# Kernel optimization log

Hardware: AMD Instinct MI355X
Metric: run time of the kernel (lower is better)

## Reference

```python
import jax, jax.numpy as jnp
import numpy as np

B, S, D, H, F = 4, 4096, 1024, 16, 4096
CAP = 0.125
ROPE_BASE = 10000.0


def setup_inputs() -> dict:
    key = jax.random.key(0)
    ks = jax.random.split(key, 9)
    scale = 0.02
    x = jax.random.normal(ks[0], (B, S, D), jnp.float32)
    causal = jnp.where(jnp.tril(jnp.ones((S, S), bool)), 0.0, -1e9).astype(jnp.float32)
    attention_mask = jnp.broadcast_to(causal[None, None], (B, 1, S, S))
    position_ids = jnp.broadcast_to(jnp.arange(S, dtype=jnp.int32), (B, S))
    return {
        "x": x,
        "attention_mask": attention_mask,
        "position_ids": position_ids,
        "router_w": jax.random.normal(ks[1], (D, 1), jnp.float32) * scale,
        "router_b": jnp.zeros((1,), jnp.float32),
        "wq": jax.random.normal(ks[2], (D, D), jnp.float32) * scale,
        "wk": jax.random.normal(ks[3], (D, D), jnp.float32) * scale,
        "wv": jax.random.normal(ks[4], (D, D), jnp.float32) * scale,
        "wo": jax.random.normal(ks[5], (D, D), jnp.float32) * scale,
        "w1": jax.random.normal(ks[6], (D, F), jnp.float32) * scale,
        "w2": jax.random.normal(ks[7], (F, D), jnp.float32) * scale,
        "ln1": jnp.ones((D,), jnp.float32),
        "ln2": jnp.ones((D,), jnp.float32),
    }


def rmsnorm(x, g):
    return x * jax.lax.rsqrt(jnp.mean(x * x, -1, keepdims=True) + 1e-6) * g


def rope(t, pos):
    # t: [b, h, n, hd], pos: [b, n]
    hd = t.shape[-1]
    inv = 1.0 / (ROPE_BASE ** (jnp.arange(0, hd, 2, dtype=jnp.float32) / hd))
    f = pos[:, None, :, None].astype(jnp.float32) * inv  # [b,1,n,hd/2]
    emb = jnp.concatenate([f, f], axis=-1)
    cos, sin = jnp.cos(emb), jnp.sin(emb)
    rot = jnp.concatenate([-t[..., hd // 2:], t[..., : hd // 2]], axis=-1)
    return t * cos + rot * sin


def reference(x, attention_mask, position_ids, router_w, router_b,
              wq, wk, wv, wo, w1, w2, ln1, ln2):
    b, s, d = x.shape
    hd = d // H
    # router
    weights = (x @ router_w)[..., 0] + router_b[0]  # [b,s]
    k = int(CAP * s)
    topv, topi = jax.lax.top_k(weights, k)
    thr = topv[:, -1]
    sel_mask = (weights > thr[:, None]).astype(x.dtype)  # selects k-1 tokens/row
    kc = k - 1
    sel_idx = jnp.sort(topi[:, :kc], axis=1)  # preserve sequence order, [b,kc]
    bidx = jnp.arange(b)[:, None]
    # gather selected tokens / positions / weights
    x_sel = x[bidx, sel_idx]                 # [b,kc,d]
    pos_sel = position_ids[bidx, sel_idx]    # [b,kc]
    w_sel = weights[bidx, sel_idx]           # [b,kc]
    m = attention_mask[:, 0]                 # [b,s,s]
    m_sel = m[bidx[:, :, None], sel_idx[:, :, None], sel_idx[:, None, :]]  # [b,kc,kc]
    # transformer block on selected tokens
    hn = rmsnorm(x_sel, ln1)

    def heads(t):
        return t.reshape(b, kc, H, hd).transpose(0, 2, 1, 3)

    q = rope(heads(hn @ wq), pos_sel)
    kk = rope(heads(hn @ wk), pos_sel)
    v = heads(hn @ wv)
    sc = jnp.einsum('bhqd,bhkd->bhqk', q, kk) / np.sqrt(hd).astype(np.float32)
    sc = sc + m_sel[:, None]
    a = jax.nn.softmax(sc, axis=-1)
    o = jnp.einsum('bhqk,bhkd->bhqd', a, v).transpose(0, 2, 1, 3).reshape(b, kc, d) @ wo
    x1 = x_sel + o
    x2 = x1 + jax.nn.gelu(rmsnorm(x1, ln2) @ w1) @ w2
    # weighted scatter back + residual passthrough for unselected tokens
    proc = x2 * w_sel[..., None]
    out = jnp.zeros_like(x).at[bidx, sel_idx].set(proc)
    return out + x * (1.0 - sel_mask)[..., None]
```

## Files before the change

### kernel.cpp

```cpp
#include <hip/hip_runtime.h>

typedef __bf16 bf16;
typedef __bf16 bf16x8 __attribute__((ext_vector_type(8)));
typedef __bf16 bf16x4 __attribute__((ext_vector_type(4)));
typedef float f32x4 __attribute__((ext_vector_type(4)));

#define B_ 4
#define S_ 4096
#define D_ 1024
#define H_ 16
#define HD_ 64
#define F_ 4096
#define KC 512
#define M_ (B_ * KC)

#define GLDS16(gp, lp)                                                        \
    __builtin_amdgcn_global_load_lds(                                         \
        (const __attribute__((address_space(1))) void*)(gp),                  \
        (__attribute__((address_space(3))) void*)(lp), 16, 0, 0)

__global__ __launch_bounds__(256) void prep_kernel(const float* __restrict__ x,
                                                   const float* __restrict__ rw,
                                                   const float* __restrict__ rb,
                                                   float* __restrict__ weights,
                                                   const float* __restrict__ wq, bf16* __restrict__ wqT,
                                                   const float* __restrict__ wk, bf16* __restrict__ wkT,
                                                   const float* __restrict__ wv, bf16* __restrict__ wvT,
                                                   const float* __restrict__ wo, bf16* __restrict__ woT,
                                                   const float* __restrict__ w1, bf16* __restrict__ w1T,
                                                   const float* __restrict__ w2, bf16* __restrict__ w2T) {
    int bid = blockIdx.x;
    if (bid < 4096) {
        int wvv = threadIdx.x >> 6, lane = threadIdx.x & 63;
        int t = bid * 4 + wvv;
        const float* xr = x + (size_t)t * D_;
        float s = 0.f;
        for (int c = 0; c < 4; c++) {
            int off = c * 256 + lane * 4;
            float4 xv = *(const float4*)(xr + off);
            float4 wv4 = *(const float4*)(rw + off);
            s += xv.x * wv4.x + xv.y * wv4.y + xv.z * wv4.z + xv.w * wv4.w;
        }
        for (int m = 32; m; m >>= 1) s += __shfl_down(s, m);
        if (lane == 0) weights[t] = s + rb[0];
        return;
    }
    bid -= 4096;
    const float* in;
    bf16* out;
    int C, R, bx, by;
    if (bid < 1024)      { in = wq; out = wqT; C = 1024; R = 1024; bx = bid & 31; by = bid >> 5; }
    else if (bid < 2048) { int t = bid - 1024; in = wk; out = wkT; C = 1024; R = 1024; bx = t & 31; by = t >> 5; }
    else if (bid < 3072) { int t = bid - 2048; in = wv; out = wvT; C = 1024; R = 1024; bx = t & 31; by = t >> 5; }
    else if (bid < 4096) { int t = bid - 3072; in = wo; out = woT; C = 1024; R = 1024; bx = t & 31; by = t >> 5; }
    else if (bid < 8192) { int t = bid - 4096; in = w1; out = w1T; C = 4096; R = 1024; bx = t & 127; by = t >> 7; }
    else                 { int t = bid - 8192; in = w2; out = w2T; C = 1024; R = 4096; bx = t & 31; by = t >> 5; }
    __shared__ bf16 tile[32][33];
    int tx = threadIdx.x & 31, ty = threadIdx.x >> 5;
    int c0 = bx * 32, r0 = by * 32;
    for (int k = 0; k < 4; k++)
        tile[ty + k * 8][tx] = (bf16)in[(size_t)(r0 + ty + k * 8) * C + c0 + tx];
    __syncthreads();
    for (int k = 0; k < 4; k++)
        out[(size_t)(c0 + ty + k * 8) * R + r0 + tx] = tile[tx][ty + k * 8];
}

__global__ __launch_bounds__(1024) void topk_kernel(const float* __restrict__ weights,
                                                    const int* __restrict__ pos_ids,
                                                    int* __restrict__ sel_idx,
                                                    float* __restrict__ w_sel,
                                                    float* __restrict__ possel,
                                                    float* __restrict__ thr,
                                                    int* __restrict__ invmap) {
    __shared__ unsigned ords[S_];
    __shared__ unsigned hist[16][256];
    __shared__ unsigned wscan[16];
    __shared__ unsigned found[2];
    int b = blockIdx.x, tid = threadIdx.x, wv = tid >> 6, lane = tid & 63;
    const float* wb = weights + (size_t)b * S_;
    for (int i = tid; i < S_; i += 1024) {
        unsigned bits = __float_as_uint(wb[i]);
        ords[i] = (bits & 0x80000000u) ? ~bits : (bits | 0x80000000u);
        invmap[b * S_ + i] = -1;
    }
    unsigned pref = 0, pmask = 0;
    int rank = 512;
    for (int level = 0; level < 4; level++) {
        int shift = 24 - level * 8;
        for (int i = tid; i < 16 * 256; i += 1024) (&hist[0][0])[i] = 0;
        __syncthreads();
        for (int i = tid; i < S_; i += 1024) {
            unsigned o = ords[i];
            if ((o & pmask) == pref) atomicAdd(&hist[wv][(o >> shift) & 255], 1u);
        }
        __syncthreads();
        unsigned val = 0, v = 0;
        if (tid < 256) {
            unsigned s = 0;
            for (int w = 0; w < 16; w++) s += hist[w][255 - tid];
            val = s;
            v = s;
            for (int d = 1; d < 64; d <<= 1) {
                unsigned u = __shfl_up(v, d);
                if (lane >= d) v += u;
            }
            if (lane == 63) wscan[wv] = v;
        }
        __syncthreads();
        if (tid < 256) {
            unsigned woff = 0;
            for (int w = 0; w < wv; w++) woff += wscan[w];
            unsigned Ccnt = v + woff;
            if (val > 0 && Ccnt >= (unsigned)rank && Ccnt - val < (unsigned)rank) {
                found[0] = 255 - (unsigned)tid;
                found[1] = Ccnt - val;
            }
        }
        __syncthreads();
        pref |= found[0] << shift;
        pmask |= 0xffu << shift;
        rank -= (int)found[1];
        __syncthreads();
    }
    unsigned T = pref;
    int need_eq = rank - 1;
    unsigned cnt = 0;
    int i0 = tid * 4;
    unsigned o4[4];
    for (int k = 0; k < 4; k++) {
        unsigned o = ords[i0 + k];
        o4[k] = o;
        cnt += (o > T) ? 1u : 0u;
        cnt += (o == T) ? 0x10000u : 0u;
    }
    unsigned v2 = cnt;
    for (int d = 1; d < 64; d <<= 1) {
        unsigned u = __shfl_up(v2, d);
        if (lane >= d) v2 += u;
    }
    if (lane == 63) wscan[wv] = v2;
    __syncthreads();
    unsigned woff2 = 0;
    for (int w = 0; w < wv; w++) woff2 += wscan[w];
    unsigned excl = woff2 + v2 - cnt;
    unsigned gbe = excl & 0xffffu, ebe = excl >> 16;
    for (int k = 0; k < 4; k++) {
        unsigned o = o4[k];
        bool gt = o > T, eq = (o == T);
        if (gt || (eq && ebe < (unsigned)need_eq)) {
            unsigned esel = (ebe < (unsigned)need_eq) ? ebe : (unsigned)need_eq;
            unsigned pos = gbe + esel;
            sel_idx[b * KC + pos] = i0 + k;
            w_sel[b * KC + pos] = wb[i0 + k];
            possel[b * KC + pos] = (float)pos_ids[b * S_ + i0 + k];
            invmap[b * S_ + i0 + k] = (int)pos;
        }
        gbe += gt ? 1u : 0u;
        ebe += eq ? 1u : 0u;
    }
    if (tid == 0) {
        unsigned bits = (T & 0x80000000u) ? (T & 0x7fffffffu) : ~T;
        thr[b] = __uint_as_float(bits);
        sel_idx[b * KC + 511] = 0;
        w_sel[b * KC + 511] = 0.0f;
        possel[b * KC + 511] = 0.0f;
    }
}

__global__ __launch_bounds__(256) void gather_norm_kernel(const float* __restrict__ x,
                                                          const int* __restrict__ sel_idx,
                                                          const float* __restrict__ ln1,
                                                          bf16* __restrict__ hn) {
    int r = blockIdx.x, b = r >> 9, j = r & (KC - 1);
    int tid = threadIdx.x;
    bf16* outr = hn + (size_t)r * D_;
    if (j == 511) {
        ((uint2*)outr)[tid] = make_uint2(0u, 0u);
        return;
    }
    int idx = sel_idx[r];
    const float* xr = x + ((size_t)b * S_ + idx) * D_;
    float4 xv = ((const float4*)xr)[tid];
    float v[4] = {xv.x, xv.y, xv.z, xv.w}, ss = 0.f;
    for (int i = 0; i < 4; i++) ss += v[i] * v[i];
    __shared__ float red[4];
    float t = ss;
    for (int m = 32; m; m >>= 1) t += __shfl_down(t, m);
    if ((tid & 63) == 0) red[tid >> 6] = t;
    __syncthreads();
    ss = red[0] + red[1] + red[2] + red[3];
    float scale = rsqrtf(ss * (1.0f / D_) + 1e-6f);
    float4 lv = ((const float4*)ln1)[tid];
    float lg[4] = {lv.x, lv.y, lv.z, lv.w};
    bf16x4 o;
    for (int i = 0; i < 4; i++) o[i] = (bf16)(v[i] * scale * lg[i]);
    ((bf16x4*)outr)[tid] = o;
}

template <bool GELU, bool ROPE, typename OUT>
__global__ __launch_bounds__(256) void gemm_bt(const bf16* __restrict__ A,
                                               const bf16* __restrict__ B0,
                                               const bf16* __restrict__ B1,
                                               const bf16* __restrict__ B2,
                                               OUT* __restrict__ C, int K, int lda,
                                               int N, int mat_shift,
                                               const float* __restrict__ possel) {
    __shared__ bf16 As[3][128 * 32];
    __shared__ bf16 Bs[3][128 * 32];
    unsigned h = blockIdx.x + gridDim.x * (blockIdx.y + gridDim.y * blockIdx.z);
    unsigned Nb = gridDim.x * gridDim.y * gridDim.z;
    unsigned cpx = Nb >> 3;
    unsigned L = (h & 7) * cpx + (h >> 3);
    unsigned by = L & 15;
    unsigned rest = L >> 4;
    unsigned bxu = rest % gridDim.x;
    unsigned bzu = rest / gridDim.x;
    int m0 = by * 128, n0 = bxu * 128;
    int kz = bzu * K;
    int tid = threadIdx.x;
    int wave = tid >> 6, lane = tid & 63, quad = lane >> 4, l16 = lane & 15;
    int wm = (wave >> 1) * 64, wn = (wave & 1) * 64;
    int mat = n0 >> mat_shift;
    const bf16* bp = (mat == 0) ? B0 : ((mat == 1) ? B1 : B2);
    int nb = n0 - (mat << mat_shift);
    int r0 = tid >> 2;
    int ksw = ((tid & 3) ^ ((tid >> 3) & 3)) * 8;
    const bf16* a0 = A + (size_t)(m0 + r0) * lda + kz + ksw;
    const bf16* a1 = A + (size_t)(m0 + r0 + 64) * lda + kz + ksw;
    const bf16* bq0 = bp + (size_t)(nb + r0) * lda + kz + ksw;
    const bf16* bq1 = bp + (size_t)(nb + r0 + 64) * lda + kz + ksw;
    int nk = K >> 5;
#define STAGE_T(buf, kk)                                                      \
    do {                                                                      \
        int ks = (kk) << 5;                                                   \
        GLDS16(a0 + ks, &As[buf][tid * 8]);                                   \
        GLDS16(a1 + ks, &As[buf][2048 + tid * 8]);                            \
        GLDS16(bq0 + ks, &Bs[buf][tid * 8]);                                  \
        GLDS16(bq1 + ks, &Bs[buf][2048 + tid * 8]);                           \
    } while (0)
    STAGE_T(0, 0);
    STAGE_T(1, 1);
    f32x4 acc[4][4] = {};
    int qsw = (quad ^ ((l16 >> 1) & 3)) * 8;
    int cur = 0, pf = 2;
    for (int t = 0; t < nk; t++) {
        if (t + 2 < nk) {
            STAGE_T(pf, t + 2);
            asm volatile("s_waitcnt vmcnt(8)\n\ts_barrier" ::: "memory");
        } else if (t + 1 < nk) {
            asm volatile("s_waitcnt vmcnt(4)\n\ts_barrier" ::: "memory");
        } else {
            asm volatile("s_waitcnt vmcnt(0)\n\ts_barrier" ::: "memory");
        }
        const bf16* Ac = &As[cur][0];
        const bf16* Bc = &Bs[cur][0];
        bf16x8 af[4], bfr[4];
        for (int tt = 0; tt < 4; tt++)
            af[tt] = *(const bf16x8*)(Ac + (wm + tt * 16 + l16) * 32 + qsw);
        for (int tt = 0; tt < 4; tt++)
            bfr[tt] = *(const bf16x8*)(Bc + (wn + tt * 16 + l16) * 32 + qsw);
        for (int tm = 0; tm < 4; tm++)
            for (int tn = 0; tn < 4; tn++)
                acc[tm][tn] = __builtin_amdgcn_mfma_f32_16x16x32_bf16(af[tm], bfr[tn], acc[tm][tn], 0, 0, 0);
        asm volatile("s_barrier" ::: "memory");
        cur = (cur == 2) ? 0 : cur + 1;
        pf = (pf == 2) ? 0 : pf + 1;
    }
#undef STAGE_T
    if (ROPE && n0 < 2048) {
        float inv0 = expf(-0.28782313662425572f * (float)l16);
        float inv1 = expf(-0.28782313662425572f * (float)(16 + l16));
        for (int tm = 0; tm < 4; tm++)
            for (int r = 0; r < 4; r++) {
                int rowg = m0 + wm + tm * 16 + quad * 4 + r;
                float pos = possel[rowg];
                {
                    float f = pos * inv0, cs = cosf(f), sn = sinf(f);
                    float lo = acc[tm][0][r], hi = acc[tm][2][r];
                    acc[tm][0][r] = lo * cs - hi * sn;
                    acc[tm][2][r] = hi * cs + lo * sn;
                }
                {
                    float f = pos * inv1, cs = cosf(f), sn = sinf(f);
                    float lo = acc[tm][1][r], hi = acc[tm][3][r];
                    acc[tm][1][r] = lo * cs - hi * sn;
                    acc[tm][3][r] = hi * cs + lo * sn;
                }
            }
    }
    C += (size_t)bzu * 2048 * N;
    for (int tm = 0; tm < 4; tm++)
        for (int tn = 0; tn < 4; tn++) {
            int col = n0 + wn + tn * 16 + l16;
            for (int r = 0; r < 4; r++) {
                int row = m0 + wm + tm * 16 + quad * 4 + r;
                float v = acc[tm][tn][r];
                if (GELU) {
                    float x3 = v * v * v;
                    v = 0.5f * v * (1.f + tanhf(0.7978845608028654f * (v + 0.044715f * x3)));
                }
                C[(size_t)row * N + col] = (OUT)v;
            }
        }
}

__global__ __launch_bounds__(256) void attn_kernel(const bf16* __restrict__ qkv,
                                                   bf16* __restrict__ O) {
    __shared__ bf16 Qs[64 * 72];
    __shared__ bf16 Ks[64 * 72];
    __shared__ bf16 Vts[64 * 72];
    __shared__ bf16 Ps[64 * 72];
    int bid = blockIdx.x;
    int bh = bid & 63;
    int qt = ((bid >> 6) & 3) | ((bid >> 8) << 2);
    int bb = bh >> 4, hh = bh & 15;
    int q_base = qt * 64;
    int tid = threadIdx.x, wave = tid >> 6, lane = tid & 63, quad = lane >> 4, l16 = lane & 15;
    const bf16* qg = qkv + ((size_t)(bb * KC + q_base)) * 3072 + hh * HD_;
    for (int i = 0; i < 2; i++) {
        int c = tid * 2 + i, row = c >> 3, ko = (c & 7) * 8;
        *(uint4*)(Qs + row * 72 + ko) = *(const uint4*)(qg + (size_t)row * 3072 + ko);
    }
    f32x4 oacc[4] = {};
    float mrow[4], lrow[4];
    for (int r = 0; r < 4; r++) { mrow[r] = -1e30f; lrow[r] = 0.f; }
    for (int kt = 0; kt <= qt; kt++) {
        __syncthreads();
        const bf16* kg = qkv + ((size_t)(bb * KC + kt * 64)) * 3072 + D_ + hh * HD_;
        for (int i = 0; i < 2; i++) {
            int c = tid * 2 + i, row = c >> 3, ko = (c & 7) * 8;
            *(uint4*)(Ks + row * 72 + ko) = *(const uint4*)(kg + (size_t)row * 3072 + ko);
        }
        const bf16* vbase = qkv + ((size_t)(bb * KC + kt * 64)) * 3072 + 2 * D_ + hh * HD_;
        for (int p = 0; p < 2; p++) {
            int jj = p * 32 + (tid >> 3), ko = (tid & 7) * 8;
            bf16x8 vv = *(const bf16x8*)(vbase + (size_t)jj * 3072 + ko);
            int colp = (((jj >> 3) ^ (tid & 7)) << 3) | (jj & 7);
            for (int e = 0; e < 8; e++) Vts[(ko + e) * 72 + colp] = vv[e];
        }
        __syncthreads();
        f32x4 sacc[4] = {};
        for (int kk = 0; kk < 2; kk++) {
            bf16x8 aq = *(const bf16x8*)(Qs + (wave * 16 + l16) * 72 + kk * 32 + quad * 8);
            for (int tn = 0; tn < 4; tn++) {
                bf16x8 bk = *(const bf16x8*)(Ks + (tn * 16 + l16) * 72 + kk * 32 + quad * 8);
                sacc[tn] = __builtin_amdgcn_mfma_f32_16x16x32_bf16(aq, bk, sacc[tn], 0, 0, 0);
            }
        }
        for (int r = 0; r < 4; r++) {
            int qi = q_base + wave * 16 + quad * 4 + r;
            float sv[4], mx = -1e30f;
            for (int tn = 0; tn < 4; tn++) {
                int kj = kt * 64 + tn * 16 + l16;
                float s = sacc[tn][r] * 0.125f;
                if (kj > qi) s = -1e30f;
                sv[tn] = s;
                mx = fmaxf(mx, s);
            }
            for (int m = 1; m < 16; m <<= 1) mx = fmaxf(mx, __shfl_xor(mx, m));
            float mnew = fmaxf(mrow[r], mx);
            float alpha = __expf(mrow[r] - mnew);
            float rs = 0.f;
            for (int tn = 0; tn < 4; tn++) {
                float pv = __expf(sv[tn] - mnew);
                rs += pv;
                Ps[(wave * 16 + quad * 4 + r) * 72 + tn * 16 + l16] = (bf16)pv;
            }
            for (int m = 1; m < 16; m <<= 1) rs += __shfl_xor(rs, m);
            lrow[r] = lrow[r] * alpha + rs;
            mrow[r] = mnew;
            for (int tn = 0; tn < 4; tn++) oacc[tn][r] *= alpha;
        }
        __syncthreads();
        for (int kk = 0; kk < 2; kk++) {
            bf16x8 ap = *(const bf16x8*)(Ps + (wave * 16 + l16) * 72 + kk * 32 + quad * 8);
            for (int tn = 0; tn < 4; tn++) {
                int d = tn * 16 + l16;
                int colb = (((kk * 4 + quad) ^ ((d >> 3) & 7)) << 3);
                bf16x8 bv = *(const bf16x8*)(Vts + d * 72 + colb);
                oacc[tn] = __builtin_amdgcn_mfma_f32_16x16x32_bf16(ap, bv, oacc[tn], 0, 0, 0);
            }
        }
    }
    for (int tn = 0; tn < 4; tn++)
        for (int r = 0; r < 4; r++) {
            int rowg = bb * KC + q_base + wave * 16 + quad * 4 + r;
            int col = hh * HD_ + tn * 16 + l16;
            O[(size_t)rowg * D_ + col] = (bf16)(oacc[tn][r] / lrow[r]);
        }
}

__global__ __launch_bounds__(256) void x1norm_kernel(const float* __restrict__ x,
                                                     const bf16* __restrict__ wo_out,
                                                     const int* __restrict__ sel_idx,
                                                     const float* __restrict__ ln2,
                                                     bf16* __restrict__ h_in) {
    int r = blockIdx.x, b = r >> 9;
    int idx = sel_idx[r];
    int tid = threadIdx.x;
    const float* xr = x + ((size_t)b * S_ + idx) * D_;
    float4 xv = ((const float4*)xr)[tid];
    bf16x4 ov = ((const bf16x4*)(wo_out + (size_t)r * D_))[tid];
    float v[4] = {xv.x + (float)ov[0], xv.y + (float)ov[1], xv.z + (float)ov[2], xv.w + (float)ov[3]};
    float ss = 0.f;
    for (int i = 0; i < 4; i++) ss += v[i] * v[i];
    __shared__ float red[4];
    float t = ss;
    for (int m = 32; m; m >>= 1) t += __shfl_down(t, m);
    if ((tid & 63) == 0) red[tid >> 6] = t;
    __syncthreads();
    ss = red[0] + red[1] + red[2] + red[3];
    float scale = rsqrtf(ss * (1.0f / D_) + 1e-6f);
    float4 lv = ((const float4*)ln2)[tid];
    float lg[4] = {lv.x, lv.y, lv.z, lv.w};
    bf16x4 o;
    for (int i = 0; i < 4; i++) o[i] = (bf16)(v[i] * scale * lg[i]);
    ((bf16x4*)(h_in + (size_t)r * D_))[tid] = o;
}

__global__ __launch_bounds__(256) void out_fused_kernel(const float* __restrict__ x,
                                                        const bf16* __restrict__ wo_out,
                                                        const float* __restrict__ f2a,
                                                        const float* __restrict__ f2b,
                                                        const int* __restrict__ invmap,
                                                        const float* __restrict__ weights,
                                                        const float* __restrict__ thr,
                                                        const float* __restrict__ w_sel,
                                                        float* __restrict__ out) {
    int t = blockIdx.x;
    int b = t >> 12;
    int tid = threadIdx.x;
    float w = weights[t];
    float th = thr[b];
    float4 xv = ((const float4*)(x + (size_t)t * D_))[tid];
    float4 res;
    if (w > th) { res.x = 0.f; res.y = 0.f; res.z = 0.f; res.w = 0.f; }
    else res = xv;
    int j = invmap[t];
    if (j >= 0) {
        int r = b * KC + j;
        bf16x4 wv = ((const bf16x4*)(wo_out + (size_t)r * D_))[tid];
        float4 va = ((const float4*)(f2a + (size_t)r * D_))[tid];
        float4 vb = ((const float4*)(f2b + (size_t)r * D_))[tid];
        float ws = w_sel[r];
        res.x += ((xv.x + (float)wv[0]) + (va.x + vb.x)) * ws;
        res.y += ((xv.y + (float)wv[1]) + (va.y + vb.y)) * ws;
        res.z += ((xv.z + (float)wv[2]) + (va.z + vb.z)) * ws;
        res.w += ((xv.w + (float)wv[3]) + (va.w + vb.w)) * ws;
    }
    ((float4*)(out + (size_t)t * D_))[tid] = res;
}

extern "C" void kernel_launch(void* const* d_in, const int* in_sizes, int n_in,
                              void* d_out, int out_size, void* d_ws, size_t ws_size,
                              hipStream_t stream) {
    const float* x = (const float*)d_in[0];
    const int* pos_ids = (const int*)d_in[2];
    const float* rw = (const float*)d_in[3];
    const float* rb = (const float*)d_in[4];
    const float* wq = (const float*)d_in[5];
    const float* wk = (const float*)d_in[6];
    const float* wv = (const float*)d_in[7];
    const float* wo = (const float*)d_in[8];
    const float* w1 = (const float*)d_in[9];
    const float* w2 = (const float*)d_in[10];
    const float* ln1 = (const float*)d_in[11];
    const float* ln2 = (const float*)d_in[12];
    float* out = (float*)d_out;
    (void)in_sizes; (void)n_in; (void)out_size;

    constexpr size_t MB = 1ull << 20;
    char* scr = (ws_size >= 88 * MB) ? (char*)d_ws : (char*)d_in[1];
    float* weights = (float*)(scr + 0);
    float* thr     = (float*)(scr + 0x10000);
    int*   sel     = (int*)  (scr + 0x14000);
    float* wsel    = (float*)(scr + 0x18000);
    float* possel  = (float*)(scr + 0x1A000);
    int*   invmap  = (int*)  (scr + 0x20000);
    bf16*  hn      = (bf16*) (scr + 1 * MB);
    bf16*  wqT     = (bf16*) (scr + 5 * MB);
    bf16*  wkT     = (bf16*) (scr + 7 * MB);
    bf16*  wvT     = (bf16*) (scr + 9 * MB);
    bf16*  qkv     = (bf16*) (scr + 11 * MB);
    bf16*  obuf    = (bf16*) (scr + 23 * MB);
    bf16*  woT     = (bf16*) (scr + 27 * MB);
    bf16*  wo_out  = (bf16*) (scr + 29 * MB);
    bf16*  h_in    = (bf16*) (scr + 33 * MB);
    bf16*  w1T     = (bf16*) (scr + 37 * MB);
    bf16*  h1      = (bf16*) (scr + 45 * MB);
    bf16*  w2T     = (bf16*) (scr + 61 * MB);
    float* f2a     = (float*)(scr + 69 * MB);
    float* f2b     = (float*)(scr + 77 * MB);

    prep_kernel<<<dim3(16384), 256, 0, stream>>>(x, rw, rb, weights,
                                                 wq, wqT, wk, wkT, wv, wvT,
                                                 wo, woT, w1, w1T, w2, w2T);
    topk_kernel<<<dim3(B_), 1024, 0, stream>>>(weights, pos_ids, sel, wsel, possel, thr, invmap);
    gather_norm_kernel<<<dim3(M_), 256, 0, stream>>>(x, sel, ln1, hn);
    gemm_bt<false, true, bf16><<<dim3(24, 16), 256, 0, stream>>>(hn, wqT, wkT, wvT, qkv,
                                                                 1024, 1024, 3 * D_, 10, possel);
    attn_kernel<<<dim3(512), 256, 0, stream>>>(qkv, obuf);
    gemm_bt<false, false, bf16><<<dim3(8, 16), 256, 0, stream>>>(obuf, woT, woT, woT, wo_out,
                                                                 1024, 1024, D_, 10, nullptr);
    x1norm_kernel<<<dim3(M_), 256, 0, stream>>>(x, wo_out, sel, ln2, h_in);
    gemm_bt<true, false, bf16><<<dim3(32, 16), 256, 0, stream>>>(h_in, w1T, w1T, w1T, h1,
                                                                 1024, 1024, F_, 12, nullptr);
    gemm_bt<false, false, float><<<dim3(8, 16, 2), 256, 0, stream>>>(h1, w2T, w2T, w2T, f2a,
                                                                     2048, 4096, D_, 10, nullptr);
    out_fused_kernel<<<dim3(B_ * S_), 256, 0, stream>>>(x, wo_out, f2a, f2b, invmap,
                                                        weights, thr, wsel, out);
}
```

Baseline: 591.5 us.

## Split-K the Wo and W2 GEMMs to raise block count, summing partials downstream

The Wo projection becomes a 2-way split-K GEMM that writes fp32 partials, and the W2 GEMM goes from 2-way to 4-way split-K. The partials are summed inside the x1norm and fused output kernels. This raises the number of workgroups for these small-M GEMMs so more compute units stay busy. In exchange it adds fp32 partial-buffer traffic and a larger scratch requirement (116 MB), and the Wo output is now kept in fp32 rather than rounded to bf16.

After: 580.7 us. No clear change (-1.8%).

```diff
diff --git a/kernel.cpp b/kernel.cpp
--- a/kernel.cpp
+++ b/kernel.cpp
@@ -391,7 +391,7 @@
 }
 
 __global__ __launch_bounds__(256) void x1norm_kernel(const float* __restrict__ x,
-                                                     const bf16* __restrict__ wo_out,
+                                                     const float* __restrict__ woacc,
                                                      const int* __restrict__ sel_idx,
                                                      const float* __restrict__ ln2,
                                                      bf16* __restrict__ h_in) {
@@ -400,8 +400,10 @@
     int tid = threadIdx.x;
     const float* xr = x + ((size_t)b * S_ + idx) * D_;
     float4 xv = ((const float4*)xr)[tid];
-    bf16x4 ov = ((const bf16x4*)(wo_out + (size_t)r * D_))[tid];
-    float v[4] = {xv.x + (float)ov[0], xv.y + (float)ov[1], xv.z + (float)ov[2], xv.w + (float)ov[3]};
+    float4 oa = ((const float4*)(woacc + (size_t)r * D_))[tid];
+    float4 ob = ((const float4*)(woacc + (size_t)2048 * D_ + (size_t)r * D_))[tid];
+    float v[4] = {xv.x + oa.x + ob.x, xv.y + oa.y + ob.y,
+                  xv.z + oa.z + ob.z, xv.w + oa.w + ob.w};
     float ss = 0.f;
     for (int i = 0; i < 4; i++) ss += v[i] * v[i];
     __shared__ float red[4];
@@ -419,9 +421,8 @@
 }
 
 __global__ __launch_bounds__(256) void out_fused_kernel(const float* __restrict__ x,
-                                                        const bf16* __restrict__ wo_out,
-                                                        const float* __restrict__ f2a,
-                                                        const float* __restrict__ f2b,
+                                                        const float* __restrict__ woacc,
+                                                        const float* __restrict__ f2,
                                                         const int* __restrict__ invmap,
                                                         const float* __restrict__ weights,
                                                         const float* __restrict__ thr,
@@ -439,14 +440,19 @@
     int j = invmap[t];
     if (j >= 0) {
         int r = b * KC + j;
-        bf16x4 wv = ((const bf16x4*)(wo_out + (size_t)r * D_))[tid];
-        float4 va = ((const float4*)(f2a + (size_t)r * D_))[tid];
-        float4 vb = ((const float4*)(f2b + (size_t)r * D_))[tid];
+        float4 oa = ((const float4*)(woacc + (size_t)r * D_))[tid];
+        float4 ob = ((const float4*)(woacc + (size_t)2048 * D_ + (size_t)r * D_))[tid];
+        float wox = oa.x + ob.x, woy = oa.y + ob.y, woz = oa.z + ob.z, wow = oa.w + ob.w;
+        float fsx = 0.f, fsy = 0.f, fsz = 0.f, fsw = 0.f;
+        for (int s = 0; s < 4; s++) {
+            float4 vf = ((const float4*)(f2 + (size_t)s * 2048 * D_ + (size_t)r * D_))[tid];
+            fsx += vf.x; fsy += vf.y; fsz += vf.z; fsw += vf.w;
+        }
         float ws = w_sel[r];
-        res.x += ((xv.x + (float)wv[0]) + (va.x + vb.x)) * ws;
-        res.y += ((xv.y + (float)wv[1]) + (va.y + vb.y)) * ws;
-        res.z += ((xv.z + (float)wv[2]) + (va.z + vb.z)) * ws;
-        res.w += ((xv.w + (float)wv[3]) + (va.w + vb.w)) * ws;
+        res.x += ((xv.x + wox) + fsx) * ws;
+        res.y += ((xv.y + woy) + fsy) * ws;
+        res.z += ((xv.z + woz) + fsz) * ws;
+        res.w += ((xv.w + wow) + fsw) * ws;
     }
     ((float4*)(out + (size_t)t * D_))[tid] = res;
 }
@@ -470,7 +476,7 @@
     (void)in_sizes; (void)n_in; (void)out_size;
 
     constexpr size_t MB = 1ull << 20;
-    char* scr = (ws_size >= 88 * MB) ? (char*)d_ws : (char*)d_in[1];
+    char* scr = (ws_size >= 116 * MB) ? (char*)d_ws : (char*)d_in[1];
     float* weights = (float*)(scr + 0);
     float* thr     = (float*)(scr + 0x10000);
     int*   sel     = (int*)  (scr + 0x14000);
@@ -484,13 +490,12 @@
     bf16*  qkv     = (bf16*) (scr + 11 * MB);
     bf16*  obuf    = (bf16*) (scr + 23 * MB);
     bf16*  woT     = (bf16*) (scr + 27 * MB);
-    bf16*  wo_out  = (bf16*) (scr + 29 * MB);
-    bf16*  h_in    = (bf16*) (scr + 33 * MB);
-    bf16*  w1T     = (bf16*) (scr + 37 * MB);
-    bf16*  h1      = (bf16*) (scr + 45 * MB);
-    bf16*  w2T     = (bf16*) (scr + 61 * MB);
-    float* f2a     = (float*)(scr + 69 * MB);
-    float* f2b     = (float*)(scr + 77 * MB);
+    float* woacc   = (float*)(scr + 29 * MB);
+    bf16*  h_in    = (bf16*) (scr + 45 * MB);
+    bf16*  w1T     = (bf16*) (scr + 49 * MB);
+    bf16*  h1      = (bf16*) (scr + 57 * MB);
+    bf16*  w2T     = (bf16*) (scr + 73 * MB);
+    float* f2      = (float*)(scr + 81 * MB);
 
     prep_kernel<<<dim3(16384), 256, 0, stream>>>(x, rw, rb, weights,
                                                  wq, wqT, wk, wkT, wv, wvT,
@@ -500,13 +505,13 @@
     gemm_bt<false, true, bf16><<<dim3(24, 16), 256, 0, stream>>>(hn, wqT, wkT, wvT, qkv,
                                                                  1024, 1024, 3 * D_, 10, possel);
     attn_kernel<<<dim3(512), 256, 0, stream>>>(qkv, obuf);
-    gemm_bt<false, false, bf16><<<dim3(8, 16), 256, 0, stream>>>(obuf, woT, woT, woT, wo_out,
-                                                                 1024, 1024, D_, 10, nullptr);
-    x1norm_kernel<<<dim3(M_), 256, 0, stream>>>(x, wo_out, sel, ln2, h_in);
+    gemm_bt<false, false, float><<<dim3(8, 16, 2), 256, 0, stream>>>(obuf, woT, woT, woT, woacc,
+                                                                     512, 1024, D_, 10, nullptr);
+    x1norm_kernel<<<dim3(M_), 256, 0, stream>>>(x, woacc, sel, ln2, h_in);
     gemm_bt<true, false, bf16><<<dim3(32, 16), 256, 0, stream>>>(h_in, w1T, w1T, w1T, h1,
                                                                  1024, 1024, F_, 12, nullptr);
-    gemm_bt<false, false, float><<<dim3(8, 16, 2), 256, 0, stream>>>(h1, w2T, w2T, w2T, f2a,
-                                                                     2048, 4096, D_, 10, nullptr);
-    out_fused_kernel<<<dim3(B_ * S_), 256, 0, stream>>>(x, wo_out, f2a, f2b, invmap,
+    gemm_bt<false, false, float><<<dim3(8, 16, 4), 256, 0, stream>>>(h1, w2T, w2T, w2T, f2,
+                                                                     1024, 4096, D_, 10, nullptr);
+    out_fused_kernel<<<dim3(B_ * S_), 256, 0, stream>>>(x, woacc, f2, invmap,
                                                         weights, thr, wsel, out);
 }
```
